# Performance work log

Hardware: AMD Instinct MI355X
Metric: run time of the kernel (lower is better)

Reference implementation:

```python
import jax, jax.numpy as jnp
import numpy as np

WS = 7           # window_size
NUM_HEADS = 4
DIM = 128
BNW = 4096       # batch * num_windows
NW = 64          # windows per image (attn_mask leading dim)
N = WS * WS      # tokens per window = 49


def make_rel_idx(ws: int) -> np.ndarray:
    coords = np.stack(np.meshgrid(np.arange(ws), np.arange(ws), indexing='ij'))  # (2, ws, ws)
    flat = coords.reshape(2, -1)                                                  # (2, N)
    rel = flat[:, :, None] - flat[:, None, :]                                     # (2, N, N)
    rel = rel.transpose(1, 2, 0).copy()
    rel[:, :, 0] += ws - 1
    rel[:, :, 1] += ws - 1
    rel[:, :, 0] *= 2 * ws - 1
    return rel.sum(-1).astype(np.int32)                                           # (N, N)


def setup_inputs() -> dict:
    key = jax.random.key(0)
    ks = jax.random.split(key, 4)
    x = jax.random.normal(ks[0], (BNW, N, DIM), dtype=jnp.float32)
    attn_mask = jnp.zeros((NW, N, N), dtype=jnp.float32)
    qkv_w = jax.random.normal(ks[1], (3 * DIM, DIM), dtype=jnp.float32) * 0.02
    qkv_b = jnp.zeros((3 * DIM,), dtype=jnp.float32)
    proj_w = jax.random.normal(ks[2], (DIM, DIM), dtype=jnp.float32) * 0.02
    proj_b = jnp.zeros((DIM,), dtype=jnp.float32)
    bias_table = jax.random.normal(ks[3], ((2 * WS - 1) ** 2, NUM_HEADS), dtype=jnp.float32) * 0.02
    rel_idx = jnp.asarray(make_rel_idx(WS))
    return {"x": x, "attn_mask": attn_mask, "qkv_w": qkv_w, "qkv_b": qkv_b,
            "proj_w": proj_w, "proj_b": proj_b, "bias_table": bias_table,
            "rel_idx": rel_idx}


def reference(x, attn_mask, qkv_w, qkv_b, proj_w, proj_b, bias_table, rel_idx):
    BnW, n, C = x.shape
    H = NUM_HEADS
    hd = C // H
    scale = hd ** -0.5
    # qkv projection: (BnW, n, 3C) -> (3, BnW, H, n, hd)
    qkv = (x @ qkv_w.T + qkv_b).reshape(BnW, n, 3, H, hd).transpose(2, 0, 3, 1, 4)
    q, k, v = qkv[0], qkv[1], qkv[2]
    attn = jnp.einsum('bhnd,bhmd->bhnm', q * scale, k)          # (BnW, H, n, n)
    bias = bias_table[rel_idx]                                   # (n, n, H)
    attn = attn + bias.transpose(2, 0, 1)[None]                  # broadcast (1, H, n, n)
    nW = attn_mask.shape[0]
    attn = attn.reshape(-1, nW, H, n, n) + attn_mask[None, :, None]
    attn = attn.reshape(-1, H, n, n)
    attn = jax.nn.softmax(attn, axis=-1)
    out = jnp.einsum('bhnm,bhmd->bhnd', attn, v)                 # (BnW, H, n, hd)
    out = out.transpose(0, 2, 1, 3).reshape(BnW, n, C)
    return out @ proj_w.T + proj_b
```

## Files before the change

kernel.cpp:

```cpp
#include <hip/hip_runtime.h>

#define NT   49
#define HD   32
#define NH   4
#define DIM  128
#define SCALEQ 0.17677669529663687f

typedef __attribute__((ext_vector_type(8))) short short8;
typedef __attribute__((ext_vector_type(4))) short short4v;
typedef __attribute__((ext_vector_type(4))) float floatx4;
typedef short8 short8a __attribute__((may_alias));
typedef short4v short4a __attribute__((may_alias));
typedef unsigned long long ulla __attribute__((may_alias));
typedef unsigned long long ull;

__device__ __forceinline__ short f2b(float f) {
    union { float f; unsigned u; } v; v.f = f;
    return (short)((v.u + 0x7fffu + ((v.u >> 16) & 1u)) >> 16);
}
__device__ __forceinline__ ull pk4(float a, float b, float c, float d) {
    return  (ull)(unsigned short)f2b(a)
         | ((ull)(unsigned short)f2b(b) << 16)
         | ((ull)(unsigned short)f2b(c) << 32)
         | ((ull)(unsigned short)f2b(d) << 48);
}
__device__ __forceinline__ short4v pack4(floatx4 a) {
    short4v r;
    r[0] = f2b(a[0]); r[1] = f2b(a[1]); r[2] = f2b(a[2]); r[3] = f2b(a[3]);
    return r;
}
__device__ __forceinline__ float b2f(short s) {
    union { unsigned u; float f; } v; v.u = ((unsigned)(unsigned short)s) << 16;
    return v.f;
}

#if __has_builtin(__builtin_amdgcn_mfma_f32_16x16x16bf16_1k)
__device__ __forceinline__ floatx4 MFMA16(short4v a, short4v b, floatx4 c) {
    return __builtin_amdgcn_mfma_f32_16x16x16bf16_1k(a, b, c, 0, 0, 0);
}
#else
__device__ __forceinline__ floatx4 MFMA16(short4v a, short4v b, floatx4 c) {
    short8 a8 = {a[0], a[1], a[2], a[3], 0, 0, 0, 0};
    short8 b8 = {b[0], b[1], b[2], b[3], 0, 0, 0, 0};
    return __builtin_amdgcn_mfma_f32_16x16x32_bf16(a8, b8, c, 0, 0, 0);
}
#endif

__global__ __launch_bounds__(256) void wmsa_prep(
        const float* __restrict__ qkvw, const float* __restrict__ projw,
        const float* __restrict__ btab, const int* __restrict__ ridx,
        const float* __restrict__ mask,
        short* __restrict__ wqkv, short* __restrict__ wproj,
        short* __restrict__ cmb) {
    __shared__ __align__(16) int   s_ridx[NT * NT];
    __shared__ __align__(16) float s_btab[169 * 4];
    __shared__ __align__(16) float s_mask[NT * NT];

    const int wdw = blockIdx.x;
    const int tid = threadIdx.x;

    {
        int g = wdw * 256 + tid;
        const float* src = (g < 12288) ? (qkvw + g * 4) : (projw + (g - 12288) * 4);
        float4 v = *(const float4*)src;
        float s = (g < 4096) ? SCALEQ : 1.0f;
        ull pk = pk4(v.x * s, v.y * s, v.z * s, v.w * s);
        if (g < 12288) *(ulla*)(wqkv + g * 4) = pk;
        else           *(ulla*)(wproj + (g - 12288) * 4) = pk;
    }

    for (int i = tid; i < NT * NT; i += 256) s_ridx[i] = ridx[i];
    for (int i = tid; i < 169 * 4; i += 256) s_btab[i] = btab[i];
    {
        const float* mw = mask + (size_t)wdw * NT * NT;
        for (int i = tid; i < NT * NT; i += 256) s_mask[i] = mw[i];
    }
    __syncthreads();

    #pragma unroll
    for (int gi = 0; gi < 4; ++gi) {
        int g = gi * 256 + tid;
        int cc = g & 15, qq = (g >> 4) & 3, tile = g >> 6;
        int it = tile >> 2, jt = tile & 3;
        int col = jt * 16 + cc;
        int rowb = it * 16 + qq * 4;
        if (col >= NT) {
            ull m16 = (unsigned short)f2b(-1e30f);
            ull pk = m16 | (m16 << 16) | (m16 << 32) | (m16 << 48);
            #pragma unroll
            for (int h = 0; h < NH; ++h)
                *(ulla*)(cmb + (((size_t)wdw * NH + h) << 12) + g * 4) = pk;
        } else {
            float bt[4][4], mv[4];
            #pragma unroll
            for (int r = 0; r < 4; ++r) {
                int row = rowb + r;
                if (row >= NT) {
                    bt[r][0] = bt[r][1] = bt[r][2] = bt[r][3] = 0.f;
                    mv[r] = 0.f;
                } else {
                    int ri = s_ridx[row * NT + col];
                    float4 b4 = *(const float4*)(s_btab + ri * 4);
                    bt[r][0] = b4.x; bt[r][1] = b4.y; bt[r][2] = b4.z; bt[r][3] = b4.w;
                    mv[r] = s_mask[row * NT + col];
                }
            }
            #pragma unroll
            for (int h = 0; h < NH; ++h) {
                ull pk = pk4(bt[0][h] + mv[0], bt[1][h] + mv[1],
                             bt[2][h] + mv[2], bt[3][h] + mv[3]);
                *(ulla*)(cmb + (((size_t)wdw * NH + h) << 12) + g * 4) = pk;
            }
        }
    }
}

#define RWAVE 8192
#define OSTR  136
#define LDSB  32768

__global__ __launch_bounds__(256, 3) void wmsa_main(
    const float* __restrict__ x,
    const float* __restrict__ qkvb, const float* __restrict__ projb,
    const short* __restrict__ wqkv, const short* __restrict__ wproj,
    const short* __restrict__ cmb, float* __restrict__ out)
{
    __shared__ __align__(16) char pool[LDSB];
    short* lds = (short*)pool;

    const int b    = blockIdx.x;
    const int wdw  = b & 63;
    const int tid  = threadIdx.x;
    const int wave = tid >> 6;
    const int lane = tid & 63;
    const int qq   = lane >> 4;
    const int cc   = lane & 15;
    const int ccl  = cc & 7, cch = cc >> 3, cm3 = cc & 3;

    const int colbase = wave * 32 + cc;

    {
        const float* xb = x + (size_t)b * NT * DIM;
        for (int i = tid; i < NT * 32; i += 256) {
            int t = i >> 5, c4 = (i & 31) << 2;
            float4 v = *(const float4*)(xb + t * DIM + c4);
            *(ulla*)(lds + t * 136 + c4) = pk4(v.x, v.y, v.z, v.w);
        }
        for (int i = tid; i < (64 - NT) * 32; i += 256) {
            int t = NT + (i >> 5), c4 = (i & 31) << 2;
            *(ulla*)(lds + t * 136 + c4) = 0ull;
        }
    }
    __syncthreads();

    short8 af[4][4];
    #pragma unroll
    for (int it = 0; it < 4; ++it)
        #pragma unroll
        for (int ks = 0; ks < 4; ++ks)
            af[it][ks] = *(const short8a*)(lds + (it * 16 + cc) * 136 + ks * 32 + qq * 8);
    __syncthreads();

    short* pw = (short*)(pool + wave * RWAVE);

    short4v qt[2][4], kt[2][4], vq[2][4];

    #pragma unroll
    for (int jt6 = 0; jt6 < 6; ++jt6) {
        const int sec = jt6 >> 1, hlf = jt6 & 1;
        short8 bfc[4];
        {
            const int cn = sec * DIM + colbase + hlf * 16;
            #pragma unroll
            for (int ks = 0; ks < 4; ++ks)
                bfc[ks] = *(const short8a*)(wqkv + cn * DIM + ks * 32 + qq * 8);
        }
        if (sec < 2) {
            float4 b4 = *(const float4*)(qkvb + sec * DIM + wave * 32 + hlf * 16 + qq * 4);
            if (sec == 0) { b4.x *= SCALEQ; b4.y *= SCALEQ; b4.z *= SCALEQ; b4.w *= SCALEQ; }
            const floatx4 cinit = {b4.x, b4.y, b4.z, b4.w};
            #pragma unroll
            for (int tt = 0; tt < 4; ++tt) {
                floatx4 acc = cinit;
                #pragma unroll
                for (int ks = 0; ks < 4; ++ks)
                    acc = __builtin_amdgcn_mfma_f32_16x16x32_bf16(bfc[ks], af[tt][ks], acc, 0, 0, 0);
                if (sec == 0) qt[hlf][tt] = pack4(acc); else kt[hlf][tt] = pack4(acc);
            }
        } else {
            float bvv = qkvb[2 * DIM + colbase + hlf * 16];
            const floatx4 cinit = {bvv, bvv, bvv, bvv};
            #pragma unroll
            for (int it = 0; it < 4; ++it) {
                floatx4 acc = cinit;
                #pragma unroll
                for (int ks = 0; ks < 4; ++ks)
                    acc = __builtin_amdgcn_mfma_f32_16x16x32_bf16(af[it][ks], bfc[ks], acc, 0, 0, 0);
                vq[hlf][it] = pack4(acc);
            }
        }
    }

    short4v cm[16];
    {
        const short* cw = cmb + (((size_t)wdw * NH + wave) << 12);
        #pragma unroll
        for (int t16 = 0; t16 < 16; ++t16)
            cm[t16] = *(const short4a*)(cw + t16 * 256 + qq * 64 + cc * 4);
    }

    #pragma unroll
    for (int it = 0; it < 4; ++it) {
        floatx4 s[4];
        #pragma unroll
        for (int jt = 0; jt < 4; ++jt) {
            short4v cb = cm[it * 4 + jt];
            floatx4 ci = {b2f(cb.x), b2f(cb.y), b2f(cb.z), b2f(cb.w)};
            ci = MFMA16(qt[0][it], kt[0][jt], ci);
            s[jt] = MFMA16(qt[1][it], kt[1][jt], ci);
        }
        #pragma unroll
        for (int r = 0; r < 4; ++r) {
            int t = it * 16 + qq * 4 + r;
            #pragma unroll
            for (int jt = 0; jt < 4; ++jt) {
                float ee = __expf(s[jt][r]);
                int g = (jt * 2 + cch) ^ r ^ ((qq & 1) << 2);
                pw[t * 64 + (g << 3) + ccl] = f2b(ee);
            }
        }
    }
    __asm__ volatile("" ::: "memory");

    floatx4 o[2][4];
    const short BONE = (short)0x3F80;
    const short4v ones4 = {BONE, BONE, BONE, BONE};
    #pragma unroll
    for (int tt = 0; tt < 4; ++tt) {
        short4v ptb[4];
        #pragma unroll
        for (int kt4 = 0; kt4 < 4; ++kt4) {
            int g = (kt4 * 2 + (qq >> 1)) ^ cm3 ^ (((cc >> 2) & 1) << 2);
            ptb[kt4] = *(const short4a*)(pw + (tt * 16 + cc) * 64 + (g << 3) + (qq & 1) * 4);
        }
        floatx4 a0 = {0.f, 0.f, 0.f, 0.f}, a1 = a0, sm = a0;
        #pragma unroll
        for (int kt4 = 0; kt4 < 4; ++kt4) {
            a0 = MFMA16(vq[0][kt4], ptb[kt4], a0);
            a1 = MFMA16(vq[1][kt4], ptb[kt4], a1);
            sm = MFMA16(ones4, ptb[kt4], sm);
        }
        float inv = 1.0f / sm[0];
        #pragma unroll
        for (int r = 0; r < 4; ++r) { a0[r] *= inv; a1[r] *= inv; }
        o[0][tt] = a0; o[1][tt] = a1;
    }

    short8 pcur[4], pnxt[4];
    float pbv[8];
    #pragma unroll
    for (int ks = 0; ks < 4; ++ks) {
        pcur[ks] = *(const short8a*)(wproj + cc * DIM + ks * 32 + qq * 8);
        pnxt[ks] = *(const short8a*)(wproj + (16 + cc) * DIM + ks * 32 + qq * 8);
    }
    #pragma unroll
    for (int j = 0; j < 8; ++j) pbv[j] = projb[j * 16 + cc];

    __syncthreads();

    short* ow = (short*)pool;
    #pragma unroll
    for (int hlf = 0; hlf < 2; ++hlf)
        #pragma unroll
        for (int tt = 0; tt < 4; ++tt) {
            int t  = tt * 16 + cc;
            int f0 = wave * 32 + hlf * 16 + qq * 4;
            *(ulla*)(ow + t * OSTR + f0) =
                pk4(o[hlf][tt][0], o[hlf][tt][1], o[hlf][tt][2], o[hlf][tt][3]);
        }
    __syncthreads();

    {
        short8 a2[4];
        #pragma unroll
        for (int ks = 0; ks < 4; ++ks)
            a2[ks] = *(const short8a*)(ow + (wave * 16 + cc) * OSTR + ks * 32 + qq * 8);
        float* outb = out + (size_t)b * NT * DIM;
        #pragma unroll
        for (int jt = 0; jt < 8; ++jt) {
            short8 pfut[4];
            if (jt < 6) {
                int cn = (jt + 2) * 16 + cc;
                #pragma unroll
                for (int ks = 0; ks < 4; ++ks)
                    pfut[ks] = *(const short8a*)(wproj + cn * DIM + ks * 32 + qq * 8);
            }
            float pb = pbv[jt];
            floatx4 acc = {pb, pb, pb, pb};
            #pragma unroll
            for (int ks = 0; ks < 4; ++ks)
                acc = __builtin_amdgcn_mfma_f32_16x16x32_bf16(a2[ks], pcur[ks], acc, 0, 0, 0);
            int col = jt * 16 + cc;
            #pragma unroll
            for (int r = 0; r < 4; ++r) {
                int row = wave * 16 + qq * 4 + r;
                if (row < NT) outb[row * DIM + col] = acc[r];
            }
            #pragma unroll
            for (int ks = 0; ks < 4; ++ks) { pcur[ks] = pnxt[ks]; pnxt[ks] = pfut[ks]; }
        }
    }
}

extern "C" void kernel_launch(void* const* d_in, const int* in_sizes, int n_in,
                              void* d_out, int out_size, void* d_ws, size_t ws_size,
                              hipStream_t stream) {
    const float* x     = (const float*)d_in[0];
    const float* mask  = (const float*)d_in[1];
    const float* qkvw  = (const float*)d_in[2];
    const float* qkvb  = (const float*)d_in[3];
    const float* projw = (const float*)d_in[4];
    const float* projb = (const float*)d_in[5];
    const float* btab  = (const float*)d_in[6];
    const int*   ridx  = (const int*)d_in[7];
    float* outp = (float*)d_out;

    short* wqkv  = (short*)d_ws;
    short* wproj = (short*)((char*)d_ws + 98304);
    short* cmb   = (short*)((char*)d_ws + 131072);

    wmsa_prep<<<64, 256, 0, stream>>>(qkvw, projw, btab, ridx, mask, wqkv, wproj, cmb);
    wmsa_main<<<4096, 256, 0, stream>>>(x, qkvb, projb, wqkv, wproj, cmb, outp);
}
```

Measured before the change: 308.4 us.

## Stage Q/K through LDS and use K=32 MFMA for scores, raise occupancy

Q and K projections are now computed in the same orientation as V and written to per-wave LDS as swizzled bf16, then reloaded as short8 fragments. The QK^T score computation can then use a single 16x16x32 MFMA per tile instead of two 16x16x16 MFMAs. The per-column qkv biases are hoisted into registers. Launch bounds go from 3 to 4 blocks per CU, cutting register pressure to raise occupancy, at the cost of extra LDS traffic and possible register spills.

```diff
diff --git a/kernel.cpp b/kernel.cpp
--- a/kernel.cpp
+++ b/kernel.cpp
@@ -119,7 +119,7 @@
 #define OSTR  136
 #define LDSB  32768
 
-__global__ __launch_bounds__(256, 3) void wmsa_main(
+__global__ __launch_bounds__(256, 4) void wmsa_main(
     const float* __restrict__ x,
     const float* __restrict__ qkvb, const float* __restrict__ projb,
     const short* __restrict__ wqkv, const short* __restrict__ wproj,
@@ -138,6 +138,10 @@
     const int ccl  = cc & 7, cch = cc >> 3, cm3 = cc & 3;
 
     const int colbase = wave * 32 + cc;
+    float biasv[6];
+    #pragma unroll
+    for (int j = 0; j < 6; ++j)
+        biasv[j] = qkvb[(j >> 1) * DIM + colbase + (j & 1) * 16];
 
     {
         const float* xb = x + (size_t)b * NT * DIM;
@@ -161,9 +165,11 @@
             af[it][ks] = *(const short8a*)(lds + (it * 16 + cc) * 136 + ks * 32 + qq * 8);
     __syncthreads();
 
-    short* pw = (short*)(pool + wave * RWAVE);
-
-    short4v qt[2][4], kt[2][4], vq[2][4];
+    short* qw = (short*)(pool + wave * RWAVE);
+    short* kw = qw + 2048;
+    short* pw = qw;
+
+    short4v vq[2][4];
 
     #pragma unroll
     for (int jt6 = 0; jt6 < 6; ++jt6) {
@@ -175,28 +181,25 @@
             for (int ks = 0; ks < 4; ++ks)
                 bfc[ks] = *(const short8a*)(wqkv + cn * DIM + ks * 32 + qq * 8);
         }
-        if (sec < 2) {
-            float4 b4 = *(const float4*)(qkvb + sec * DIM + wave * 32 + hlf * 16 + qq * 4);
-            if (sec == 0) { b4.x *= SCALEQ; b4.y *= SCALEQ; b4.z *= SCALEQ; b4.w *= SCALEQ; }
-            const floatx4 cinit = {b4.x, b4.y, b4.z, b4.w};
-            #pragma unroll
-            for (int tt = 0; tt < 4; ++tt) {
-                floatx4 acc = cinit;
+        float bias = biasv[jt6];
+        if (sec == 0) bias *= SCALEQ;
+        const floatx4 cinit = {bias, bias, bias, bias};
+        #pragma unroll
+        for (int it = 0; it < 4; ++it) {
+            floatx4 acc = cinit;
+            #pragma unroll
+            for (int ks = 0; ks < 4; ++ks)
+                acc = __builtin_amdgcn_mfma_f32_16x16x32_bf16(af[it][ks], bfc[ks], acc, 0, 0, 0);
+            if (sec == 2) {
+                vq[hlf][it] = pack4(acc);
+            } else {
+                short* dst = (sec == 0) ? qw : kw;
+                int gb = hlf * 2 + cch;
                 #pragma unroll
-                for (int ks = 0; ks < 4; ++ks)
-                    acc = __builtin_amdgcn_mfma_f32_16x16x32_bf16(bfc[ks], af[tt][ks], acc, 0, 0, 0);
-                if (sec == 0) qt[hlf][tt] = pack4(acc); else kt[hlf][tt] = pack4(acc);
-            }
-        } else {
-            float bvv = qkvb[2 * DIM + colbase + hlf * 16];
-            const floatx4 cinit = {bvv, bvv, bvv, bvv};
-            #pragma unroll
-            for (int it = 0; it < 4; ++it) {
-                floatx4 acc = cinit;
-                #pragma unroll
-                for (int ks = 0; ks < 4; ++ks)
-                    acc = __builtin_amdgcn_mfma_f32_16x16x32_bf16(af[it][ks], bfc[ks], acc, 0, 0, 0);
-                vq[hlf][it] = pack4(acc);
+                for (int r = 0; r < 4; ++r) {
+                    int t = it * 16 + qq * 4 + r;
+                    dst[t * 32 + ((gb ^ r) << 3) + ccl] = f2b(acc[r]);
+                }
             }
         }
     }
@@ -208,25 +211,33 @@
         for (int t16 = 0; t16 < 16; ++t16)
             cm[t16] = *(const short4a*)(cw + t16 * 256 + qq * 64 + cc * 4);
     }
-
-    #pragma unroll
-    for (int it = 0; it < 4; ++it) {
-        floatx4 s[4];
-        #pragma unroll
-        for (int jt = 0; jt < 4; ++jt) {
-            short4v cb = cm[it * 4 + jt];
-            floatx4 ci = {b2f(cb.x), b2f(cb.y), b2f(cb.z), b2f(cb.w)};
-            ci = MFMA16(qt[0][it], kt[0][jt], ci);
-            s[jt] = MFMA16(qt[1][it], kt[1][jt], ci);
-        }
-        #pragma unroll
-        for (int r = 0; r < 4; ++r) {
-            int t = it * 16 + qq * 4 + r;
+    __asm__ volatile("" ::: "memory");
+
+    {
+        short8 qf[4], kf[4];
+        #pragma unroll
+        for (int t = 0; t < 4; ++t) {
+            qf[t] = *(const short8a*)(qw + (t * 16 + cc) * 32 + ((qq ^ cm3) << 3));
+            kf[t] = *(const short8a*)(kw + (t * 16 + cc) * 32 + ((qq ^ cm3) << 3));
+        }
+        #pragma unroll
+        for (int it = 0; it < 4; ++it) {
+            floatx4 s[4];
             #pragma unroll
             for (int jt = 0; jt < 4; ++jt) {
-                float ee = __expf(s[jt][r]);
-                int g = (jt * 2 + cch) ^ r ^ ((qq & 1) << 2);
-                pw[t * 64 + (g << 3) + ccl] = f2b(ee);
+                short4v cb = cm[it * 4 + jt];
+                floatx4 ci = {b2f(cb.x), b2f(cb.y), b2f(cb.z), b2f(cb.w)};
+                s[jt] = __builtin_amdgcn_mfma_f32_16x16x32_bf16(qf[it], kf[jt], ci, 0, 0, 0);
+            }
+            #pragma unroll
+            for (int r = 0; r < 4; ++r) {
+                int t = it * 16 + qq * 4 + r;
+                #pragma unroll
+                for (int jt = 0; jt < 4; ++jt) {
+                    float ee = __expf(s[jt][r]);
+                    int g = (jt * 2 + cch) ^ r ^ ((qq & 1) << 2);
+                    pw[t * 64 + (g << 3) + ccl] = f2b(ee);
+                }
             }
         }
     }
```

New measurement: 295.1 us. 1.04x faster.
